# Kernel tuning notes

Measured on AMD Instinct MI355X. Metric: run time of the kernel, lower is better.

The kernel has to match this reference:

```python
import jax, jax.numpy as jnp
import numpy as np

INIT_MEAN = 0.3


def _loo_sum(x, idx, n_seg):
    # leave-one-out segment sum along edge axis; x: [B, E]
    tot = jnp.zeros((x.shape[0], n_seg), x.dtype).at[:, idx].add(x)
    return tot[:, idx] - x


def _check_node_process(x, chk_idx, n_checks):
    # 2*atanh( prod_{e' in check, e'!=e} tanh(x_e'/2) ) via log-magnitude + sign
    t = jnp.tanh(0.5 * x)
    abs_t = jnp.clip(jnp.abs(t), 1e-12, None)
    log_loo = _loo_sum(jnp.log(abs_t), chk_idx, n_checks)
    neg = (t < 0).astype(x.dtype)
    neg_loo = _loo_sum(neg, chk_idx, n_checks)
    sign = 1.0 - 2.0 * jnp.mod(neg_loo, 2.0)
    prod = jnp.clip(sign * jnp.exp(log_loo), -1.0 + 1e-7, 1.0 - 1e-7)
    return 2.0 * jnp.arctanh(prod)


def setup_inputs() -> dict:
    N, M, DV, DC, ITERS, B = 8192, 4096, 3, 6, 5, 1024
    E = N * DV
    rng = np.random.RandomState(0)
    # regular (3,6) Tanner graph: each variable has 3 edges, each check 6
    var_idx = np.repeat(np.arange(N, dtype=np.int32), DV)
    chk_idx = rng.permutation(np.repeat(np.arange(M, dtype=np.int32), DC)).astype(np.int32)
    key = jax.random.key(0)
    k1, k2, k3 = jax.random.split(key, 3)
    llr = jax.random.normal(k1, (B, N), dtype=jnp.float32)
    vnode_w = INIT_MEAN + 0.02 * jax.random.normal(k2, (ITERS, E), dtype=jnp.float32)
    cnode_w = INIT_MEAN + 0.02 * jax.random.normal(k3, (ITERS, E), dtype=jnp.float32)
    return {
        "llr": llr,
        "vnode_w": vnode_w,
        "cnode_w": cnode_w,
        "var_idx": jnp.asarray(var_idx),
        "chk_idx": jnp.asarray(chk_idx),
        "n_checks": M,
    }


def reference(llr, vnode_w, cnode_w, var_idx, chk_idx, n_checks):
    B, N = llr.shape
    iters = vnode_w.shape[0]
    scattered_llr = llr[:, var_idx]            # [B, E]
    ext = jnp.zeros_like(scattered_llr)
    outs = []
    for i in range(iters):
        a_priori = _loo_sum(ext, var_idx, N) * vnode_w[i]
        ext = _check_node_process(a_priori + scattered_llr, chk_idx, n_checks) * cnode_w[i]
        out = jnp.zeros((B, N), llr.dtype).at[:, var_idx].add(ext) + llr
        outs.append(out)
    return jnp.stack(outs)  # [iters, B, N]
```

## Files before the change

### kernel.cpp

```cpp
#include <hip/hip_runtime.h>


#define N_VARS 8192
#define M_CHK  4096
#define ITERS  5
#define BATCH  1024
#define NEDGE  (N_VARS * 3)
#define TPB    1024
#define EPT    (NEDGE / TPB)
#define VPT    (N_VARS / TPB)
#define CPT    (M_CHK / TPB)
#define CSTRIDE 7

#define LOG2E_F 1.44269504f
#define LN2_F   0.69314718f
#define M_CLIP  39.863137f
#define E_CLIP  0.99999988f

__device__ __forceinline__ float edge_msg(float x) {
    float a  = fabsf(x);
    float ee = __builtin_amdgcn_exp2f(-a * LOG2E_F);
    float m  = __builtin_amdgcn_logf(1.0f + ee) - __builtin_amdgcn_logf(1.0f - ee);
    m = fminf(m, M_CLIP);
    unsigned neg = (x < 0.0f) ? 0x80000000u : 0u;
    return __uint_as_float(__float_as_uint(m) | neg);
}

__global__ void setup_slots(const int* __restrict__ chk,
                            unsigned* __restrict__ tbl,
                            int* __restrict__ cnt) {
    int e = blockIdx.x * 256 + threadIdx.x;
    if (e < NEDGE) {
        int c = chk[e];
        int slot = atomicAdd(&cnt[c], 1);
        tbl[e] = (unsigned)(c * CSTRIDE + slot);
    }
}

__global__ void __launch_bounds__(TPB, 4)
nsp_kernel(const float* __restrict__ llr,
           const float* __restrict__ vw,
           const float* __restrict__ cw,
           const unsigned* __restrict__ tbl,
           float* __restrict__ out)
{
    __shared__ float lds_m[M_CHK * CSTRIDE];

    const int b  = blockIdx.x;
    const int t  = threadIdx.x;
    const int e0 = t * EPT;
    const int n0 = t * VPT;

    float llr_v[VPT];
    {
        const float4* p = (const float4*)(llr + (size_t)b * N_VARS + n0);
        float4 a = p[0], c = p[1];
        llr_v[0] = a.x; llr_v[1] = a.y; llr_v[2] = a.z; llr_v[3] = a.w;
        llr_v[4] = c.x; llr_v[5] = c.y; llr_v[6] = c.z; llr_v[7] = c.w;
    }

    unsigned pa[EPT / 2];
    {
        const uint4* p = (const uint4*)(tbl + e0);
#pragma unroll
        for (int k = 0; k < EPT / 4; ++k) {
            uint4 v = p[k];
            pa[2 * k]     = v.x | (v.y << 16);
            pa[2 * k + 1] = v.z | (v.w << 16);
        }
    }
#define ADDR(e) ((pa[(e) >> 1] >> (((e) & 1) * 16)) & 0xFFFFu)

    auto phaseA4 = [&](int v0, const float* cwr, const float* vwr,
                       float* op) {
        float rr[12];
#pragma unroll
        for (int q = 0; q < 12; ++q)
            rr[q] = lds_m[ADDR(3 * v0 + q)];
        float outb[4];
#pragma unroll
        for (int vv = 0; vv < 4; ++vv) {
            const int v = v0 + vv;
            float x0 = rr[3 * vv + 0] * cwr[3 * v + 0];
            float x1 = rr[3 * vv + 1] * cwr[3 * v + 1];
            float x2 = rr[3 * vv + 2] * cwr[3 * v + 2];
            float s  = x0 + x1 + x2;
            outb[vv] = s + llr_v[v];
#pragma unroll
            for (int j = 0; j < 3; ++j) {
                const int e = 3 * v + j;
                float extj = (j == 0) ? x0 : (j == 1) ? x1 : x2;
                float x = (s - extj) * vwr[e] + llr_v[v];
                lds_m[ADDR(e)] = edge_msg(x);
            }
        }
        *((float4*)(op + v0)) = make_float4(outb[0], outb[1], outb[2], outb[3]);
    };

    for (int it = 0; it < ITERS; ++it) {
        if (it == 0) {
#pragma unroll
            for (int v = 0; v < VPT; ++v) {
                float p = edge_msg(llr_v[v]);
#pragma unroll
                for (int j = 0; j < 3; ++j)
                    lds_m[ADDR(3 * v + j)] = p;
            }
        } else {
            const float* cwr = cw + (size_t)(it - 1) * NEDGE + e0;
            const float* vwr = vw + (size_t)it * NEDGE + e0;
            float* op = out + ((size_t)(it - 1) * BATCH + b) * N_VARS + n0;
            phaseA4(0, cwr, vwr, op);
            __builtin_amdgcn_sched_barrier(0);
            phaseA4(4, cwr, vwr, op);
        }
        __syncthreads();

#pragma unroll
        for (int k = 0; k < CPT; ++k) {
            const int base = (t + k * TPB) * CSTRIDE;
            unsigned u0 = __float_as_uint(lds_m[base + 0]);
            unsigned u1 = __float_as_uint(lds_m[base + 1]);
            unsigned u2 = __float_as_uint(lds_m[base + 2]);
            unsigned u3 = __float_as_uint(lds_m[base + 3]);
            unsigned u4 = __float_as_uint(lds_m[base + 4]);
            unsigned u5 = __float_as_uint(lds_m[base + 5]);
            float S = __uint_as_float(u0 & 0x7fffffffu)
                    + __uint_as_float(u1 & 0x7fffffffu)
                    + __uint_as_float(u2 & 0x7fffffffu)
                    + __uint_as_float(u3 & 0x7fffffffu)
                    + __uint_as_float(u4 & 0x7fffffffu)
                    + __uint_as_float(u5 & 0x7fffffffu);
            unsigned P = (u0 ^ u1 ^ u2 ^ u3 ^ u4 ^ u5) & 0x80000000u;
#pragma unroll
            for (int i = 0; i < 6; ++i) {
                unsigned ui = (i == 0) ? u0 : (i == 1) ? u1 : (i == 2) ? u2
                            : (i == 3) ? u3 : (i == 4) ? u4 : u5;
                float m  = __uint_as_float(ui & 0x7fffffffu);
                unsigned sg = (P ^ ui) & 0x80000000u;
                float E = __builtin_amdgcn_exp2f(m - S);
                E = fminf(E, E_CLIP);
                float r = LN2_F * (__builtin_amdgcn_logf(1.0f + E)
                                 - __builtin_amdgcn_logf(1.0f - E));
                lds_m[base + i] = __uint_as_float(__float_as_uint(r) ^ sg);
            }
        }
        __syncthreads();
    }

    {
        const float* cwr = cw + (size_t)(ITERS - 1) * NEDGE + e0;
        float* op = out + ((size_t)(ITERS - 1) * BATCH + b) * N_VARS + n0;
        auto finalF4 = [&](int v0) {
            float rr[12];
#pragma unroll
            for (int q = 0; q < 12; ++q)
                rr[q] = lds_m[ADDR(3 * v0 + q)];
            float outb[4];
#pragma unroll
            for (int vv = 0; vv < 4; ++vv) {
                const int v = v0 + vv;
                outb[vv] = rr[3 * vv + 0] * cwr[3 * v + 0]
                         + rr[3 * vv + 1] * cwr[3 * v + 1]
                         + rr[3 * vv + 2] * cwr[3 * v + 2]
                         + llr_v[v];
            }
            *((float4*)(op + v0)) = make_float4(outb[0], outb[1],
                                                outb[2], outb[3]);
        };
        finalF4(0);
        finalF4(4);
    }
#undef ADDR
}

extern "C" void kernel_launch(void* const* d_in, const int* in_sizes, int n_in,
                              void* d_out, int out_size, void* d_ws, size_t ws_size,
                              hipStream_t stream) {
    const float* llr = (const float*)d_in[0];
    const float* vw  = (const float*)d_in[1];
    const float* cw  = (const float*)d_in[2];
    const int*   chk = (const int*)d_in[4];
    float* out = (float*)d_out;

    unsigned* tbl = (unsigned*)d_ws;
    int*      cnt = (int*)((char*)d_ws + NEDGE * sizeof(unsigned));

    hipMemsetAsync(cnt, 0, M_CHK * sizeof(int), stream);
    setup_slots<<<(NEDGE + 255) / 256, 256, 0, stream>>>(chk, tbl, cnt);
    nsp_kernel<<<BATCH, TPB, 0, stream>>>(llr, vw, cw, tbl, out);
}
```

Measured before the change: 339.1 us.

## Replace log-domain check update with direct tanh prefix/suffix products

Edges now store tanh(x/2) directly, computed as (1-e)/(1+e) with a reciprocal, instead of a log-magnitude message with a packed sign. The check node forms leave-one-out products from prefix and suffix products, then applies a clamped atanh. This removes one exp2 and one log per check edge and one log per variable edge. The cost is a reciprocal per variable edge. The risk is precision loss when products underflow for large magnitudes, where the old log-domain sum was more robust.

```diff
diff --git a/kernel.cpp b/kernel.cpp
--- a/kernel.cpp
+++ b/kernel.cpp
@@ -14,16 +14,20 @@
 
 #define LOG2E_F 1.44269504f
 #define LN2_F   0.69314718f
-#define M_CLIP  39.863137f
 #define E_CLIP  0.99999988f
 
-__device__ __forceinline__ float edge_msg(float x) {
+__device__ __forceinline__ float tanh_half(float x) {
     float a  = fabsf(x);
     float ee = __builtin_amdgcn_exp2f(-a * LOG2E_F);
-    float m  = __builtin_amdgcn_logf(1.0f + ee) - __builtin_amdgcn_logf(1.0f - ee);
-    m = fminf(m, M_CLIP);
-    unsigned neg = (x < 0.0f) ? 0x80000000u : 0u;
-    return __uint_as_float(__float_as_uint(m) | neg);
+    float tt = (1.0f - ee) * __builtin_amdgcn_rcpf(1.0f + ee);
+    unsigned sg = __float_as_uint(x) & 0x80000000u;
+    return __uint_as_float(__float_as_uint(tt) | sg);
+}
+
+__device__ __forceinline__ float atanh2(float p) {
+    p = fminf(fmaxf(p, -E_CLIP), E_CLIP);
+    return LN2_F * (__builtin_amdgcn_logf(1.0f + p)
+                  - __builtin_amdgcn_logf(1.0f - p));
 }
 
 __global__ void setup_slots(const int* __restrict__ chk,
@@ -91,7 +95,7 @@
                 const int e = 3 * v + j;
                 float extj = (j == 0) ? x0 : (j == 1) ? x1 : x2;
                 float x = (s - extj) * vwr[e] + llr_v[v];
-                lds_m[ADDR(e)] = edge_msg(x);
+                lds_m[ADDR(e)] = tanh_half(x);
             }
         }
         *((float4*)(op + v0)) = make_float4(outb[0], outb[1], outb[2], outb[3]);
@@ -101,7 +105,7 @@
         if (it == 0) {
 #pragma unroll
             for (int v = 0; v < VPT; ++v) {
-                float p = edge_msg(llr_v[v]);
+                float p = tanh_half(llr_v[v]);
 #pragma unroll
                 for (int j = 0; j < 3; ++j)
                     lds_m[ADDR(3 * v + j)] = p;
@@ -119,31 +123,26 @@
 #pragma unroll
         for (int k = 0; k < CPT; ++k) {
             const int base = (t + k * TPB) * CSTRIDE;
-            unsigned u0 = __float_as_uint(lds_m[base + 0]);
-            unsigned u1 = __float_as_uint(lds_m[base + 1]);
-            unsigned u2 = __float_as_uint(lds_m[base + 2]);
-            unsigned u3 = __float_as_uint(lds_m[base + 3]);
-            unsigned u4 = __float_as_uint(lds_m[base + 4]);
-            unsigned u5 = __float_as_uint(lds_m[base + 5]);
-            float S = __uint_as_float(u0 & 0x7fffffffu)
-                    + __uint_as_float(u1 & 0x7fffffffu)
-                    + __uint_as_float(u2 & 0x7fffffffu)
-                    + __uint_as_float(u3 & 0x7fffffffu)
-                    + __uint_as_float(u4 & 0x7fffffffu)
-                    + __uint_as_float(u5 & 0x7fffffffu);
-            unsigned P = (u0 ^ u1 ^ u2 ^ u3 ^ u4 ^ u5) & 0x80000000u;
-#pragma unroll
-            for (int i = 0; i < 6; ++i) {
-                unsigned ui = (i == 0) ? u0 : (i == 1) ? u1 : (i == 2) ? u2
-                            : (i == 3) ? u3 : (i == 4) ? u4 : u5;
-                float m  = __uint_as_float(ui & 0x7fffffffu);
-                unsigned sg = (P ^ ui) & 0x80000000u;
-                float E = __builtin_amdgcn_exp2f(m - S);
-                E = fminf(E, E_CLIP);
-                float r = LN2_F * (__builtin_amdgcn_logf(1.0f + E)
-                                 - __builtin_amdgcn_logf(1.0f - E));
-                lds_m[base + i] = __uint_as_float(__float_as_uint(r) ^ sg);
-            }
+            float t0 = lds_m[base + 0];
+            float t1 = lds_m[base + 1];
+            float t2 = lds_m[base + 2];
+            float t3 = lds_m[base + 3];
+            float t4 = lds_m[base + 4];
+            float t5 = lds_m[base + 5];
+            float p1 = t0 * t1;
+            float p2 = p1 * t2;
+            float p3 = p2 * t3;
+            float p4 = p3 * t4;
+            float s4 = t5 * t4;
+            float s3 = s4 * t3;
+            float s2 = s3 * t2;
+            float s1 = s2 * t1;
+            lds_m[base + 0] = atanh2(s1);
+            lds_m[base + 1] = atanh2(t0 * s2);
+            lds_m[base + 2] = atanh2(p1 * s3);
+            lds_m[base + 3] = atanh2(p2 * s4);
+            lds_m[base + 4] = atanh2(p3 * t5);
+            lds_m[base + 5] = atanh2(p4);
         }
         __syncthreads();
     }
```

Measured after the change: 321.5 us. -5.2%, faster.
